# Kernel tuning notes

Hardware: AMD Instinct MI355X
Metric: run time of the kernel (lower is better)

## Reference

```python
import jax
import jax.numpy as jnp
import numpy as np
from jax.scipy.linalg import expm

H = 2048   # hidden_size
R = 1      # low-rank dimension
B = 2048   # batch of independent (h, x) pairs


def _glorot(key, shape):
    return jax.random.uniform(key, shape, minval=-1.0, maxval=1.0) * jnp.sqrt(2.0 / sum(shape))


def setup_inputs() -> dict:
    key = jax.random.key(0)
    k1, k2, k3, k4, k5, k6 = jax.random.split(key, 6)
    return {
        "h": jax.random.normal(k5, (B, H), dtype=jnp.float32),
        "x": jax.random.normal(k6, (B, H), dtype=jnp.float32),
        # a_diag ~ U(-1, 0) * init_scale (10.0): negative real diagonal
        "a_diag": jax.random.uniform(k1, (H,), minval=-1.0, maxval=0.0) * 10.0,
        "p_vec": _glorot(k2, (H, R)),
        "q_vec": _glorot(k3, (H, R)),
        "b_mat": _glorot(k4, (H, H)),
        "delta": jnp.array(0.1, dtype=jnp.float32),
    }


def reference(h, x, a_diag, p_vec, q_vec, b_mat, delta):
    # A = diag(a_diag) + P Q^T  (DPLR structure, materialized dense as in source)
    A = jnp.diag(a_diag) + p_vec @ q_vec.T                       # [H, H]
    # Discretized state matrix: exp(delta * A)
    expA = expm(delta * A)                                       # [H, H]
    # Discretized input matrix: A^{-1} (exp(delta A) - I) B  (pinv as in source)
    A_inv = jnp.linalg.pinv(A)                                   # [H, H]
    B_disc = A_inv @ (expA - jnp.eye(H, dtype=A.dtype)) @ b_mat  # [H, H]
    # Batched recurrence step: A h + B x  for each row of h, x
    return h @ expA.T + x @ B_disc.T                             # [B, H]
```

## Files before the change

### kernel.cpp

```cpp
#include <hip/hip_runtime.h>

#define MAXM 16
#define NL_CAP 256
#define THETA 0.1f
#define SMEM_BYTES 36864

typedef unsigned short u16;
typedef u16 u16x8 __attribute__((ext_vector_type(8)));
typedef u16 u16x4 __attribute__((ext_vector_type(4)));
typedef __bf16 bf16x8 __attribute__((ext_vector_type(8)));
typedef float f32x4 __attribute__((ext_vector_type(4)));


__device__ __forceinline__ u16 f2bf(float f) {
    unsigned u = __float_as_uint(f);
    return (u16)((u + 0x7fffu + ((u >> 16) & 1u)) >> 16);
}

__global__ __launch_bounds__(256)
void conv_k(const float* __restrict__ x, const float* __restrict__ b,
            u16* __restrict__ xb, u16* __restrict__ bb, long nx, long nb)
{
    long i = ((long)blockIdx.x * 256 + threadIdx.x) * 4;
    if (i < nx) {
        float4 v = *(const float4*)&x[i];
        u16x4 o = {f2bf(v.x), f2bf(v.y), f2bf(v.z), f2bf(v.w)};
        *(u16x4*)&xb[i] = o;
    }
    if (i < nb) {
        float4 v = *(const float4*)&b[i];
        u16x4 o = {f2bf(v.x), f2bf(v.y), f2bf(v.z), f2bf(v.w)};
        *(u16x4*)&bb[i] = o;
    }
}


__device__ __forceinline__ double frcp(double den) {
    double r = (double)__builtin_amdgcn_rcpf((float)den);
    return fma(r, fma(-den, r, 1.0), r);
}


__device__ __forceinline__ void gload_lds16(const void* g, void* l) {
    __builtin_amdgcn_global_load_lds(
        (const __attribute__((address_space(1))) unsigned int*)g,
        (__attribute__((address_space(3))) unsigned int*)l, 16, 0, 0);
}

__device__ __forceinline__ void gemm_tile(u16* Al, u16* Bl, int tid, int bx, int by,
                                          const u16* __restrict__ A,
                                          const u16* __restrict__ B,
                                          float* __restrict__ C,
                                          int Ndim, int Kstride, int Klen)
{
    const int bm = by * 128, bn = bx * 128;
    const int wv = tid >> 6, ln = tid & 63;
    const int wr = (wv >> 1) * 64, wc = (wv & 1) * 64;
    const int fr = ln & 15, fk = (ln >> 4) * 8;

    const int r0 = tid >> 2, c0 = (tid & 3) * 8;
    const u16* Ap0 = A + (size_t)(bm + r0) * Kstride + c0;
    const u16* Ap1 = Ap0 + (size_t)64 * Kstride;
    const u16* Bp0 = B + (size_t)(bn + r0) * Kstride + c0;
    const u16* Bp1 = Bp0 + (size_t)64 * Kstride;
    u16* AlW0 = Al + wv * 512;
    u16* AlW1 = Al + 2048 + wv * 512;
    u16* BlW0 = Bl + wv * 512;
    u16* BlW1 = Bl + 2048 + wv * 512;

    f32x4 acc[4][4];
#pragma unroll
    for (int m = 0; m < 4; ++m)
#pragma unroll
        for (int n = 0; n < 4; ++n) acc[m][n] = (f32x4)0.f;

    for (int kk = 0; kk < Klen; kk += 32) {
        __syncthreads();
        gload_lds16(Ap0 + kk, AlW0);
        gload_lds16(Ap1 + kk, AlW1);
        gload_lds16(Bp0 + kk, BlW0);
        gload_lds16(Bp1 + kk, BlW1);
        __syncthreads();
        u16x8 af[4], bf[4];
#pragma unroll
        for (int m = 0; m < 4; ++m)
            af[m] = *(const u16x8*)&Al[(wr + m * 16 + fr) * 32 + fk];
#pragma unroll
        for (int n = 0; n < 4; ++n)
            bf[n] = *(const u16x8*)&Bl[(wc + n * 16 + fr) * 32 + fk];
#pragma unroll
        for (int m = 0; m < 4; ++m)
#pragma unroll
            for (int n = 0; n < 4; ++n)
                acc[m][n] = __builtin_amdgcn_mfma_f32_16x16x32_bf16(
                    __builtin_bit_cast(bf16x8, af[m]),
                    __builtin_bit_cast(bf16x8, bf[n]), acc[m][n], 0, 0, 0);
    }

    const int crow = (ln >> 4) * 4;
#pragma unroll
    for (int m = 0; m < 4; ++m)
#pragma unroll
        for (int n = 0; n < 4; ++n) {
            const size_t base = (size_t)(bm + wr + m * 16 + crow) * Ndim
                              + bn + wc + n * 16 + fr;
#pragma unroll
            for (int j = 0; j < 4; ++j)
                C[base + (size_t)j * Ndim] = acc[m][n][j];
        }
}

__global__ __launch_bounds__(256)
void bgemm_k(const u16* __restrict__ A, const u16* __restrict__ B,
             float* __restrict__ C, int Ndim, int Kdim)
{
    __shared__ __align__(16) unsigned char smem[SMEM_BYTES];
    gemm_tile((u16*)smem, (u16*)smem + 4096, threadIdx.x,
              blockIdx.x, blockIdx.y, A, B, C, Ndim, Kdim, Kdim);
}


__global__ __launch_bounds__(256)
void g_sgemm_k(const float* __restrict__ A, const float* __restrict__ B,
               float* __restrict__ C, int Mdim, int Ndim, int Kdim)
{
    __shared__ __align__(16) float As[16][132];
    __shared__ __align__(16) float Bs[16][68];
    const int tid = threadIdx.x;
    const int tx = tid & 15, ty = tid >> 4;
    const int bn = blockIdx.x * 64, bm = blockIdx.y * 128;
    const int lrA = tid >> 1, lcA = (tid & 1) << 3;
    const int lrB = tid >> 2, lcB = (tid & 3) << 2;
    const float* Aptr = A + (size_t)(bm + lrA) * Kdim + lcA;
    const float* Bptr = B + (size_t)(bn + lrB) * Kdim + lcB;
    float4 a0 = *(const float4*)(Aptr);
    float4 a1 = *(const float4*)(Aptr + 4);
    float4 b0 = *(const float4*)(Bptr);
    float acc[8][4];
#pragma unroll
    for (int i = 0; i < 8; ++i)
#pragma unroll
        for (int j = 0; j < 4; ++j) acc[i][j] = 0.f;
    for (int kk = 0; kk < Kdim; kk += 16) {
        __syncthreads();
        As[lcA + 0][lrA] = a0.x; As[lcA + 1][lrA] = a0.y;
        As[lcA + 2][lrA] = a0.z; As[lcA + 3][lrA] = a0.w;
        As[lcA + 4][lrA] = a1.x; As[lcA + 5][lrA] = a1.y;
        As[lcA + 6][lrA] = a1.z; As[lcA + 7][lrA] = a1.w;
        Bs[lcB + 0][lrB] = b0.x; Bs[lcB + 1][lrB] = b0.y;
        Bs[lcB + 2][lrB] = b0.z; Bs[lcB + 3][lrB] = b0.w;
        __syncthreads();
        if (kk + 16 < Kdim) {
            a0 = *(const float4*)(Aptr + kk + 16);
            a1 = *(const float4*)(Aptr + kk + 20);
            b0 = *(const float4*)(Bptr + kk + 16);
        }
#pragma unroll
        for (int k = 0; k < 16; ++k) {
            const float4 av0 = *(const float4*)&As[k][ty * 8];
            const float4 av1 = *(const float4*)&As[k][ty * 8 + 4];
            const float4 bv  = *(const float4*)&Bs[k][tx * 4];
            const float avf[8] = {av0.x, av0.y, av0.z, av0.w, av1.x, av1.y, av1.z, av1.w};
            const float bvf[4] = {bv.x, bv.y, bv.z, bv.w};
#pragma unroll
            for (int i = 0; i < 8; ++i)
#pragma unroll
                for (int j = 0; j < 4; ++j) acc[i][j] += avf[i] * bvf[j];
        }
    }
#pragma unroll
    for (int i = 0; i < 8; ++i) {
        const int r = bm + ty * 8 + i;
        float4 v = {acc[i][0], acc[i][1], acc[i][2], acc[i][3]};
        *(float4*)&C[(size_t)r * Ndim + bn + tx * 4] = v;
    }
}


__device__ __forceinline__ double wsum(double x) {
#pragma unroll
    for (int m = 32; m; m >>= 1) x += __shfl_xor(x, m, 64);
    return x;
}
__device__ __forceinline__ float wsumf(float x) {
#pragma unroll
    for (int m = 32; m; m >>= 1) x += __shfl_xor(x, m, 64);
    return x;
}

__device__ __forceinline__ int inert(double s11, double s12, double s22,
                                     double dc, double cS)
{
    double b00 = cS - s11, b01 = -1.0 - s12, b11 = -s22;
    double det = b00 * b11 - b01 * b01, tr = b00 + b11;
    int neg = (det > 0.0) ? ((tr < 0.0) ? 2 : 0) : 1;
    return (int)(dc + 0.5) + neg - 1;
}

__device__ __forceinline__ int lane_evalN32(float tf, double td, int n4,
    const float4* l0, const float4* l1, const float4* l2,
    const double* pc, bool poly, double cS,
    double& g11o, double& g12o, double& g22o)
{
    float s11 = 0.f, s12 = 0.f, s22 = 0.f, dc = 0.f;
#pragma unroll 2
    for (int i = 0; i < n4; ++i) {
        const float4 d4 = l0[i], x4 = l1[i], y4 = l2[i];
        const float dd[4] = {d4.x, d4.y, d4.z, d4.w};
        const float xx[4] = {x4.x, x4.y, x4.z, x4.w};
        const float yy[4] = {y4.x, y4.y, y4.z, y4.w};
#pragma unroll
        for (int e = 0; e < 4; ++e) {
            float den = dd[e] - tf;
            float mag = fmaxf(fabsf(den), 1e-30f);
            den = (den < 0.f) ? -mag : mag;
            const float inv = __builtin_amdgcn_rcpf(den);
            s11 = fmaf(xx[e] * xx[e], inv, s11);
            s12 = fmaf(xx[e] * yy[e], inv, s12);
            s22 = fmaf(yy[e] * yy[e], inv, s22);
            if (dd[e] < tf) dc += 1.f;
        }
    }
    double S11 = (double)s11, S12 = (double)s12, S22 = (double)s22;
    if (poly) {
        S11 += pc[0] + td * (pc[3] + td * (pc[6] + td * pc[9]));
        S12 += pc[1] + td * (pc[4] + td * (pc[7] + td * pc[10]));
        S22 += pc[2] + td * (pc[5] + td * (pc[8] + td * pc[11]));
    }
    g11o = S11; g12o = S12; g22o = S22;
    return inert(S11, S12, S22, (double)dc, cS);
}

__device__ void spec256(unsigned char* smem, int tid,
                        const float* __restrict__ av, const float* __restrict__ pv,
                        const float* __restrict__ qv, double* __restrict__ hdr,
                        float* __restrict__ V)
{
    float* sd2 = (float*)smem;
    float* sw1 = sd2 + 2048;
    float* sw2 = sw1 + 2048;
    float* nl0 = sw2 + 2048;
    float* nl1 = nl0 + NL_CAP;
    float* nl2 = nl1 + NL_CAP;
    double* dsh = (double*)(nl2 + NL_CAP);
    int* ish = (int*)(dsh + 192);

    const int lane = tid & 63, wv = tid >> 6;
    const int j0 = tid * 8;

    float d2r[8], w1r[8], w2r[8];
    double cS = 0, n1 = 0, n2 = 0, mx = 0;
#pragma unroll
    for (int h = 0; h < 2; ++h) {
        float4 aa = *(const float4*)&av[j0 + h * 4];
        float4 pp = *(const float4*)&pv[j0 + h * 4];
        float4 qq = *(const float4*)&qv[j0 + h * 4];
        const float a4[4] = {aa.x, aa.y, aa.z, aa.w};
        const float p4[4] = {pp.x, pp.y, pp.z, pp.w};
        const float q4[4] = {qq.x, qq.y, qq.z, qq.w};
#pragma unroll
        for (int e = 0; e < 4; ++e) {
            const int ix = h * 4 + e;
            d2r[ix] = a4[e] * a4[e];
            w1r[ix] = a4[e] * p4[e];
            w2r[ix] = q4[e];
            sd2[j0 + ix] = d2r[ix]; sw1[j0 + ix] = w1r[ix]; sw2[j0 + ix] = w2r[ix];
            cS += (double)p4[e] * p4[e];
            n1 += (double)w1r[ix] * w1r[ix];
            n2 += (double)w2r[ix] * w2r[ix];
            mx = fmax(mx, (double)d2r[ix]);
        }
    }
    cS = wsum(cS); n1 = wsum(n1); n2 = wsum(n2);
#pragma unroll
    for (int m_ = 32; m_; m_ >>= 1) mx = fmax(mx, __shfl_xor(mx, m_, 64));
    __syncthreads();
    if (lane == 0) { dsh[wv] = cS; dsh[4 + wv] = n1; dsh[8 + wv] = n2; dsh[12 + wv] = mx; }
    __syncthreads();
    cS = 0; n1 = 0; n2 = 0; mx = 0;
    for (int w = 0; w < 4; ++w) {
        cS += dsh[w]; n1 += dsh[4 + w]; n2 += dsh[8 + w];
        mx = fmax(mx, dsh[12 + w]);
    }
    __syncthreads();

    double lo = 0.0;
    double hi = mx + 0.5 * (cS + sqrt(cS * cS + 4.0)) * (n1 + n2) + 1.0;
    for (int r = 0; r < 8; ++r) {
        const double td = lo + (hi - lo) * (double)(wv + 1) / 5.0;
        const float tf = (float)td;
        float s11 = 0.f, s12 = 0.f, s22 = 0.f, dc = 0.f;
        for (int i4 = lane; i4 < 512; i4 += 64) {
            const float4 dd = ((const float4*)sd2)[i4];
            const float4 e1 = ((const float4*)sw1)[i4];
            const float4 e2 = ((const float4*)sw2)[i4];
            const float df[4] = {dd.x, dd.y, dd.z, dd.w};
            const float f1[4] = {e1.x, e1.y, e1.z, e1.w};
            const float f2[4] = {e2.x, e2.y, e2.z, e2.w};
#pragma unroll
            for (int e = 0; e < 4; ++e) {
                float den = df[e] - tf;
                float mag = fmaxf(fabsf(den), 1e-30f);
                den = (den < 0.f) ? -mag : mag;
                const float inv = __builtin_amdgcn_rcpf(den);
                s11 = fmaf(f1[e] * f1[e], inv, s11);
                s12 = fmaf(f1[e] * f2[e], inv, s12);
                s22 = fmaf(f2[e] * f2[e], inv, s22);
                if (df[e] < tf) dc += 1.f;
            }
        }
        s11 = wsumf(s11); s12 = wsumf(s12); s22 = wsumf(s22); dc = wsumf(dc);
        if (lane == 0)
            ish[wv] = inert((double)s11, (double)s12, (double)s22, (double)dc, cS);
        __syncthreads();
        double nlo = lo, nhi = hi;
        for (int i = 0; i < 4; ++i) {
            double ti = lo + (hi - lo) * (double)(i + 1) / 5.0;
            if (ish[i] >= 2048) { if (ti < nhi) nhi = ti; }
            else                { if (ti > nlo) nlo = ti; }
        }
        lo = nlo; hi = nhi;
        __syncthreads();
    }
    const double lmax = 0.5 * (lo + hi);
    const double rc = 10.0 * 2048.0 * 1.1920928955078125e-07;
    const double cut2 = rc * rc * lmax;

    int flags = 0, lc = 0;
#pragma unroll
    for (int e = 0; e < 8; ++e)
        if (d2r[e] < THETA) { flags |= (1 << e); ++lc; }
    int sc = lc;
#pragma unroll
    for (int off = 1; off < 64; off <<= 1) {
        int y = __shfl_up(sc, off, 64);
        if (lane >= off) sc += y;
    }
    const int wtot = __shfl(sc, 63, 64);
    const int excl = sc - lc;
    if (lane == 0) ish[4 + wv] = wtot;
    __syncthreads();
    int base = excl;
    for (int w = 0; w < wv; ++w) base += ish[4 + w];
    int cnt = 0;
    for (int w = 0; w < 4; ++w) cnt += ish[4 + w];
    {
        int pos = base;
#pragma unroll
        for (int e = 0; e < 8; ++e) {
            if (flags & (1 << e)) {
                if (pos < NL_CAP) { nl0[pos] = d2r[e]; nl1[pos] = w1r[e]; nl2[pos] = w2r[e]; }
                ++pos;
            }
        }
    }
    const int cntPad = (cnt + 7) & ~7;
    if (tid == 0) {
        for (int i = cnt; i < cntPad && i < NL_CAP; ++i) {
            nl0[i] = 1e30f; nl1[i] = 0.f; nl2[i] = 0.f;
        }
        ish[8] = cnt; ish[10] = cntPad >> 2;
    }

    double cf[12];
#pragma unroll
    for (int c = 0; c < 12; ++c) cf[c] = 0;
#pragma unroll
    for (int e = 0; e < 8; ++e) {
        if (d2r[e] >= THETA) {
            double id = frcp((double)d2r[e]);
            double b1 = (double)w1r[e], b2 = (double)w2r[e];
            double x11 = b1 * b1, x12 = b1 * b2, x22 = b2 * b2;
            double f = id;
            cf[0] += x11 * f; cf[1]  += x12 * f; cf[2]  += x22 * f; f *= id;
            cf[3] += x11 * f; cf[4]  += x12 * f; cf[5]  += x22 * f; f *= id;
            cf[6] += x11 * f; cf[7]  += x12 * f; cf[8]  += x22 * f; f *= id;
            cf[9] += x11 * f; cf[10] += x12 * f; cf[11] += x22 * f;
        }
    }
#pragma unroll
    for (int c = 0; c < 12; ++c) cf[c] = wsum(cf[c]);
    if (lane == 0) {
        double* dw = &dsh[16 + wv * 12];
#pragma unroll
        for (int c = 0; c < 12; ++c) dw[c] = cf[c];
    }
    __syncthreads();
    if (tid < 12) {
        double s = 0;
        for (int w = 0; w < 4; ++w) s += dsh[16 + w * 12 + tid];
        dsh[96 + tid] = s;
    }
    __syncthreads();

    cnt = ish[8];
    const bool nearOK = (cnt <= NL_CAP - 8);
    const float4* l0 = nearOK ? (const float4*)nl0 : (const float4*)sd2;
    const float4* l1 = nearOK ? (const float4*)nl1 : (const float4*)sw1;
    const float4* l2 = nearOK ? (const float4*)nl2 : (const float4*)sw2;
    const int n4 = nearOK ? ish[10] : 512;
    const bool poly = nearOK;
    const double* pcoef = &dsh[96];

    double zg1, zg2, zg3;
    if (wv == 0) {
        int N = lane_evalN32((float)cut2, cut2, n4, l0, l1, l2, pcoef, poly, cS,
                             zg1, zg2, zg3);
        if (lane == 0) ish[9] = N;
    }
    __syncthreads();
    int m = ish[9];
    if (m < 0) m = 0;
    if (m > MAXM) m = MAXM;

    for (int k = wv; k < m; k += 4) {
        double klo = 0.0, khi = cut2;
        for (int r = 0; r < 3; ++r) {
            const double w = khi - klo;
            const double td = klo + w * (double)(lane + 1) / 65.0;
            int N = lane_evalN32((float)td, td, n4, l0, l1, l2, pcoef, poly, cS,
                                 zg1, zg2, zg3);
            unsigned long long mask = __ballot(N >= k + 1);
            int j = (mask == 0ull) ? 64 : (__ffsll(mask) - 1);
            double nk = (j == 64) ? khi : (klo + w * (double)(j + 1) / 65.0);
            klo = klo + w * (double)j / 65.0;
            khi = nk;
        }
        const double lam = 0.5 * (klo + khi);
        double g11, g12, g22;
        lane_evalN32((float)lam, lam, n4, l0, l1, l2, pcoef, poly, cS, g11, g12, g22);
        const double m00 = 1.0 + g12, m01 = g11 + cS * g12;
        const double m10 = g22,       m11 = 1.0 + g12 + cS * g22;
        double y1, y2;
        if (m00 * m00 + m01 * m01 >= m10 * m10 + m11 * m11) { y1 = m01; y2 = -m00; }
        else                                                { y1 = m11; y2 = -m10; }
        if (lane == 0) {
            dsh[112 + 3 * k]     = lam;
            dsh[112 + 3 * k + 1] = y2;
            dsh[112 + 3 * k + 2] = y1 + cS * y2;
        }
    }
    __syncthreads();

    for (int k = 0; k < m; ++k) {
        const double lam = dsh[112 + 3 * k];
        const double z1 = dsh[112 + 3 * k + 1], z2 = dsh[112 + 3 * k + 2];
        double vr[8], pn = 0;
#pragma unroll
        for (int e = 0; e < 8; ++e) {
            double den = (double)d2r[e] - lam;
            if (fabs(den) < 1e-25) den = (den < 0 ? -1e-25 : 1e-25);
            vr[e] = ((double)w1r[e] * z1 + (double)w2r[e] * z2) * frcp(den);
            pn += vr[e] * vr[e];
        }
        pn = wsum(pn);
        if (lane == 0) dsh[160 + wv] = pn;
        __syncthreads();
        double tot = 0;
        for (int w = 0; w < 4; ++w) tot += dsh[160 + w];
        const double inv = 1.0 / sqrt(tot);
        float o0[8];
#pragma unroll
        for (int e = 0; e < 8; ++e) o0[e] = (float)(vr[e] * inv);
        *(float4*)&V[(size_t)k * 2048 + j0]     = *(float4*)&o0[0];
        *(float4*)&V[(size_t)k * 2048 + j0 + 4] = *(float4*)&o0[4];
        __syncthreads();
    }

    if (tid == 0) { hdr[0] = lmax; hdr[1] = cut2; hdr[2] = (double)m; hdr[3] = cS; }
}


__global__ __launch_bounds__(256)
void fat_k(const u16* __restrict__ A, const u16* __restrict__ B,
           float* __restrict__ C0, float* __restrict__ C1,
           int Ndim, int Kdim, int ntiles, int nbx, int nsplit,
           const float* __restrict__ av, const float* __restrict__ pv,
           const float* __restrict__ qv, double* __restrict__ hdr,
           float* __restrict__ V)
{
    __shared__ __align__(16) unsigned char smem[SMEM_BYTES];
    const int bid = blockIdx.x;
    if (bid == 0) {
        spec256(smem, threadIdx.x, av, pv, qv, hdr, V);
        return;
    }
    const int t = bid - 1;
    if (t >= ntiles * nsplit) return;
    const int ks = t / ntiles;
    const int tt = t - ks * ntiles;
    const int Klen = Kdim / nsplit;
    gemm_tile((u16*)smem, (u16*)smem + 4096, threadIdx.x,
              tt % nbx, tt / nbx,
              A + (size_t)ks * Klen, B + (size_t)ks * Klen,
              ks ? C1 : C0, Ndim, Kdim, Klen);
}


__global__ __launch_bounds__(256, 2)
void series_k(float* __restrict__ io, const float* __restrict__ io2, int addP,
              const float* __restrict__ hm,
              const float* __restrict__ qv, const float* __restrict__ pv,
              const float* __restrict__ av, const float* __restrict__ delta,
              const float* __restrict__ V, const double* __restrict__ hdr,
              int useTrunc)
{
    const int lane = threadIdx.x & 63;
    const int row = blockIdx.x * 4 + (threadIdx.x >> 6);
    const float d = delta[0];
    const int m = useTrunc ? (int)hdr[2] : 0;

    float q[32], p[32], a[32], t[32], o[32];
    float* iorow = io + (size_t)row * 2048;
    const float* io2row = io2 + (size_t)row * 2048;
#pragma unroll
    for (int cc = 0; cc < 8; ++cc) {
        const int j = cc * 256 + lane * 4;
        *(float4*)&q[cc * 4] = *(const float4*)&qv[j];
        *(float4*)&p[cc * 4] = *(const float4*)&pv[j];
        *(float4*)&a[cc * 4] = *(const float4*)&av[j];
        float4 u0 = *(const float4*)&iorow[j];
        if (addP) {
            const float4 u1 = *(const float4*)&io2row[j];
            u0.x += u1.x; u0.y += u1.y; u0.z += u1.z; u0.w += u1.w;
        }
        *(float4*)&t[cc * 4] = u0;
    }
#pragma unroll
    for (int e = 0; e < 32; ++e) o[e] = t[e];

    float cf = 1.f;
    for (int k = 1; k <= 13; ++k) {
        float s = 0.f;
#pragma unroll
        for (int e = 0; e < 32; ++e) s += t[e] * q[e];
#pragma unroll
        for (int msk = 32; msk; msk >>= 1) s += __shfl_xor(s, msk, 64);
        cf /= (float)(k + 1);
        const float ds = d * s;
#pragma unroll
        for (int e = 0; e < 32; ++e) { t[e] = d * a[e] * t[e] + ds * p[e]; o[e] += cf * t[e]; }
    }
#pragma unroll
    for (int e = 0; e < 32; ++e) o[e] *= d;

    for (int k = 0; k < m; ++k) {
        const float* vr = V + (size_t)k * 2048;
        float vk[32];
#pragma unroll
        for (int cc = 0; cc < 8; ++cc)
            *(float4*)&vk[cc * 4] = *(const float4*)&vr[cc * 256 + lane * 4];
        float s = 0.f;
#pragma unroll
        for (int e = 0; e < 32; ++e) s += o[e] * vk[e];
#pragma unroll
        for (int msk = 32; msk; msk >>= 1) s += __shfl_xor(s, msk, 64);
#pragma unroll
        for (int e = 0; e < 32; ++e) o[e] -= s * vk[e];
    }

    const float* hrow = hm + (size_t)row * 2048;
#pragma unroll
    for (int cc = 0; cc < 8; ++cc)
        *(float4*)&t[cc * 4] = *(const float4*)&hrow[cc * 256 + lane * 4];
#pragma unroll
    for (int e = 0; e < 32; ++e) o[e] += t[e];
    cf = 1.f;
    for (int k = 1; k <= 14; ++k) {
        float s = 0.f;
#pragma unroll
        for (int e = 0; e < 32; ++e) s += t[e] * q[e];
#pragma unroll
        for (int msk = 32; msk; msk >>= 1) s += __shfl_xor(s, msk, 64);
        cf /= (float)k;
        const float ds = d * s;
#pragma unroll
        for (int e = 0; e < 32; ++e) { t[e] = d * a[e] * t[e] + ds * p[e]; o[e] += cf * t[e]; }
    }
#pragma unroll
    for (int cc = 0; cc < 8; ++cc)
        *(float4*)&iorow[cc * 256 + lane * 4] = *(const float4*)&o[cc * 4];
}


extern "C" void kernel_launch(void* const* d_in, const int* in_sizes, int n_in,
                              void* d_out, int out_size, void* d_ws, size_t ws_size,
                              hipStream_t stream)
{
    const float* hmat  = (const float*)d_in[0];
    const float* xmat  = (const float*)d_in[1];
    const float* adiag = (const float*)d_in[2];
    const float* pvec  = (const float*)d_in[3];
    const float* qvec  = (const float*)d_in[4];
    const float* bmat  = (const float*)d_in[5];
    const float* delta = (const float*)d_in[6];
    float* out = (float*)d_out;

    const int H  = in_sizes[2];
    const int Bb = in_sizes[0] / H;
    const size_t SZ = (size_t)Bb * H;
    const size_t HH = (size_t)H * H;

    double* hdr = (double*)d_ws;
    float* V = (float*)(hdr + 8);
    u16* xb = (u16*)(V + (size_t)MAXM * H);
    u16* bb = xb + SZ;
    float* C1 = (float*)(bb + HH);

    const size_t needSpec  = 64 + (size_t)MAXM * H * sizeof(float);
    const size_t needFull  = needSpec + (SZ + HH) * sizeof(u16);
    const size_t needSplit = needFull + SZ * sizeof(float);
    const bool doTrunc = (H == 2048) && (ws_size >= needSpec);
    const bool doBf16  = (ws_size >= needFull) && (H % 128 == 0) && (Bb % 128 == 0);
    const bool doSplit = doBf16 && doTrunc && (ws_size >= needSplit) && (H % 64 == 0);

    dim3 blk256(256);
    const int nbx = H / 128;
    const int ntiles = nbx * (Bb / 128);

    if (doBf16) {
        const long nmax = (long)(SZ > HH ? SZ : HH);
        const int cg = (int)((nmax / 4 + 255) / 256);
        conv_k<<<cg, blk256, 0, stream>>>(xmat, bmat, xb, bb, (long)SZ, (long)HH);
        if (doTrunc) {
            const int nsplit = doSplit ? 2 : 1;
            fat_k<<<1 + ntiles * nsplit, blk256, 0, stream>>>(
                xb, bb, out, C1, H, H, ntiles, nbx, nsplit,
                adiag, pvec, qvec, hdr, V);
        } else {
            dim3 gg(nbx, Bb / 128);
            bgemm_k<<<gg, blk256, 0, stream>>>(xb, bb, out, H, H);
        }
    } else {
        if (doTrunc)
            fat_k<<<1, blk256, 0, stream>>>(nullptr, nullptr, out, nullptr,
                                            H, H, 0, 1, 1,
                                            adiag, pvec, qvec, hdr, V);
        dim3 gg(H / 64, Bb / 128);
        g_sgemm_k<<<gg, blk256, 0, stream>>>(xmat, bmat, out, Bb, H, H);
    }

    series_k<<<Bb / 4, blk256, 0, stream>>>(out, doSplit ? C1 : out,
                                            doSplit ? 1 : 0,
                                            hmat, qvec, pvec, adiag, delta,
                                            V, hdr, doTrunc ? 1 : 0);
}
```

Before: 91.22 us.

## Trim spectral solver: fewer bisection rounds, float moments, per-wave eigenvector normalization

In the block-0 spectral solver, the coarse bracketing loop drops from 8 to 5 rounds and the far-field cutoff THETA shrinks, so more eigenvalues go through the polynomial moment expansion. The moment coefficients are now accumulated in float with a hardware reciprocal instead of in double. Each wave now computes its own eigenvectors across all 2048 entries, with a wave-level norm reduction instead of a block-wide reduction and two syncthreads per eigenvector. This shortens the serial critical path of block 0 but risks lower accuracy in the eigenvalue bracketing and the moment coefficients.

New measurement: 107.3 us. 1.18x slower.

```diff
diff --git a/kernel.cpp b/kernel.cpp
--- a/kernel.cpp
+++ b/kernel.cpp
@@ -2,7 +2,7 @@
 
 #define MAXM 16
 #define NL_CAP 256
-#define THETA 0.1f
+#define THETA 0.04f
 #define SMEM_BYTES 36864
 
 typedef unsigned short u16;
@@ -286,7 +286,7 @@
 
     double lo = 0.0;
     double hi = mx + 0.5 * (cS + sqrt(cS * cS + 4.0)) * (n1 + n2) + 1.0;
-    for (int r = 0; r < 8; ++r) {
+    for (int r = 0; r < 5; ++r) {
         const double td = lo + (hi - lo) * (double)(wv + 1) / 5.0;
         const float tf = (float)td;
         float s11 = 0.f, s12 = 0.f, s22 = 0.f, dc = 0.f;
@@ -362,28 +362,28 @@
         ish[8] = cnt; ish[10] = cntPad >> 2;
     }
 
-    double cf[12];
-#pragma unroll
-    for (int c = 0; c < 12; ++c) cf[c] = 0;
+    float cff[12];
+#pragma unroll
+    for (int c = 0; c < 12; ++c) cff[c] = 0.f;
 #pragma unroll
     for (int e = 0; e < 8; ++e) {
         if (d2r[e] >= THETA) {
-            double id = frcp((double)d2r[e]);
-            double b1 = (double)w1r[e], b2 = (double)w2r[e];
-            double x11 = b1 * b1, x12 = b1 * b2, x22 = b2 * b2;
-            double f = id;
-            cf[0] += x11 * f; cf[1]  += x12 * f; cf[2]  += x22 * f; f *= id;
-            cf[3] += x11 * f; cf[4]  += x12 * f; cf[5]  += x22 * f; f *= id;
-            cf[6] += x11 * f; cf[7]  += x12 * f; cf[8]  += x22 * f; f *= id;
-            cf[9] += x11 * f; cf[10] += x12 * f; cf[11] += x22 * f;
-        }
-    }
-#pragma unroll
-    for (int c = 0; c < 12; ++c) cf[c] = wsum(cf[c]);
+            float id = __builtin_amdgcn_rcpf(d2r[e]);
+            float b1 = w1r[e], b2 = w2r[e];
+            float x11 = b1 * b1, x12 = b1 * b2, x22 = b2 * b2;
+            float f = id;
+            cff[0] += x11 * f; cff[1]  += x12 * f; cff[2]  += x22 * f; f *= id;
+            cff[3] += x11 * f; cff[4]  += x12 * f; cff[5]  += x22 * f; f *= id;
+            cff[6] += x11 * f; cff[7]  += x12 * f; cff[8]  += x22 * f; f *= id;
+            cff[9] += x11 * f; cff[10] += x12 * f; cff[11] += x22 * f;
+        }
+    }
+#pragma unroll
+    for (int c = 0; c < 12; ++c) cff[c] = wsumf(cff[c]);
     if (lane == 0) {
         double* dw = &dsh[16 + wv * 12];
 #pragma unroll
-        for (int c = 0; c < 12; ++c) dw[c] = cf[c];
+        for (int c = 0; c < 12; ++c) dw[c] = (double)cff[c];
     }
     __syncthreads();
     if (tid < 12) {
@@ -434,37 +434,37 @@
         double y1, y2;
         if (m00 * m00 + m01 * m01 >= m10 * m10 + m11 * m11) { y1 = m01; y2 = -m00; }
         else                                                { y1 = m11; y2 = -m10; }
-        if (lane == 0) {
-            dsh[112 + 3 * k]     = lam;
-            dsh[112 + 3 * k + 1] = y2;
-            dsh[112 + 3 * k + 2] = y1 + cS * y2;
-        }
-    }
-    __syncthreads();
-
-    for (int k = 0; k < m; ++k) {
-        const double lam = dsh[112 + 3 * k];
-        const double z1 = dsh[112 + 3 * k + 1], z2 = dsh[112 + 3 * k + 2];
-        double vr[8], pn = 0;
-#pragma unroll
-        for (int e = 0; e < 8; ++e) {
-            double den = (double)d2r[e] - lam;
-            if (fabs(den) < 1e-25) den = (den < 0 ? -1e-25 : 1e-25);
-            vr[e] = ((double)w1r[e] * z1 + (double)w2r[e] * z2) * frcp(den);
-            pn += vr[e] * vr[e];
+        const double z1 = y2, z2 = y1 + cS * y2;
+
+        float vtmp[32];
+        double pn = 0;
+#pragma unroll
+        for (int c = 0; c < 8; ++c) {
+            const int idx = c * 256 + lane * 4;
+            const float4 d4 = *(const float4*)&sd2[idx];
+            const float4 x4 = *(const float4*)&sw1[idx];
+            const float4 y4 = *(const float4*)&sw2[idx];
+            const float dd[4] = {d4.x, d4.y, d4.z, d4.w};
+            const float xx[4] = {x4.x, x4.y, x4.z, x4.w};
+            const float yy[4] = {y4.x, y4.y, y4.z, y4.w};
+#pragma unroll
+            for (int e = 0; e < 4; ++e) {
+                double den = (double)dd[e] - lam;
+                if (fabs(den) < 1e-25) den = (den < 0 ? -1e-25 : 1e-25);
+                double vi = ((double)xx[e] * z1 + (double)yy[e] * z2) * frcp(den);
+                pn += vi * vi;
+                vtmp[c * 4 + e] = (float)vi;
+            }
         }
         pn = wsum(pn);
-        if (lane == 0) dsh[160 + wv] = pn;
-        __syncthreads();
-        double tot = 0;
-        for (int w = 0; w < 4; ++w) tot += dsh[160 + w];
-        const double inv = 1.0 / sqrt(tot);
-        float o0[8];
-#pragma unroll
-        for (int e = 0; e < 8; ++e) o0[e] = (float)(vr[e] * inv);
-        *(float4*)&V[(size_t)k * 2048 + j0]     = *(float4*)&o0[0];
-        *(float4*)&V[(size_t)k * 2048 + j0 + 4] = *(float4*)&o0[4];
-        __syncthreads();
+        const float inv = (float)(1.0 / sqrt(pn));
+#pragma unroll
+        for (int c = 0; c < 8; ++c) {
+            const int idx = c * 256 + lane * 4;
+            float4 o = {vtmp[c * 4 + 0] * inv, vtmp[c * 4 + 1] * inv,
+                        vtmp[c * 4 + 2] * inv, vtmp[c * 4 + 3] * inv};
+            *(float4*)&V[(size_t)k * 2048 + idx] = o;
+        }
     }
 
     if (tid == 0) { hdr[0] = lmax; hdr[1] = cut2; hdr[2] = (double)m; hdr[3] = cS; }
```
